# Optimization experiments

Hardware: AMD Instinct MI355X
Metric: run time of the kernel (lower is better)

## Reference

```python
import jax, jax.numpy as jnp
import numpy as np

NUM_HEADS = 16
DIM_HEAD = 64
SCALE = DIM_HEAD ** -0.5
ROPE_BASE = 10000.0


def _rope(t):
    # t: [b, h, n, d] -> rotary embedding with rotate-half convention
    n, d = t.shape[2], t.shape[3]
    inv_freq = 1.0 / (ROPE_BASE ** (jnp.arange(0, d, 2, dtype=jnp.float32) / d))
    freqs = jnp.arange(n, dtype=jnp.float32)[:, None] * inv_freq[None, :]  # [n, d/2]
    cos = jnp.concatenate([jnp.cos(freqs), jnp.cos(freqs)], axis=-1)  # [n, d]
    sin = jnp.concatenate([jnp.sin(freqs), jnp.sin(freqs)], axis=-1)
    t1, t2 = jnp.split(t, 2, axis=-1)
    rot = jnp.concatenate([-t2, t1], axis=-1)
    return t * cos + rot * sin


def setup_inputs() -> dict:
    key = jax.random.key(0)
    k1, k2, k3 = jax.random.split(key, 3)
    B, N, D = 2, 2049, 1024  # 2048 patches + 1 cls token
    x = jax.random.normal(k1, (B, N, D), dtype=jnp.float32)
    ln_gamma = jnp.ones((D,), dtype=jnp.float32)
    ln_beta = jnp.zeros((D,), dtype=jnp.float32)
    w_qkv = jax.random.normal(k2, (D, 3 * NUM_HEADS * DIM_HEAD), dtype=jnp.float32) * 0.02
    w_out = jax.random.normal(k3, (NUM_HEADS * DIM_HEAD, D), dtype=jnp.float32) * 0.02
    return {"x": x, "ln_gamma": ln_gamma, "ln_beta": ln_beta, "w_qkv": w_qkv, "w_out": w_out}


def reference(x, ln_gamma, ln_beta, w_qkv, w_out):
    B, N, D = x.shape
    # LayerNorm (eps=1e-5, torch default)
    mu = jnp.mean(x, axis=-1, keepdims=True)
    var = jnp.mean(jnp.square(x - mu), axis=-1, keepdims=True)
    xn = (x - mu) * jax.lax.rsqrt(var + 1e-5) * ln_gamma + ln_beta
    # QKV projection (no bias)
    qkv = xn @ w_qkv  # [B, N, 3*H*Dh]
    q, k, v = jnp.split(qkv, 3, axis=-1)
    def to_heads(t):
        return t.reshape(B, N, NUM_HEADS, DIM_HEAD).transpose(0, 2, 1, 3)  # [B,H,N,Dh]
    q, k, v = to_heads(q), to_heads(k), to_heads(v)
    # cls token excluded from RoPE
    q = jnp.concatenate([q[:, :, :1, :], _rope(q[:, :, 1:, :])], axis=2)
    k = jnp.concatenate([k[:, :, :1, :], _rope(k[:, :, 1:, :])], axis=2)
    dots = jnp.einsum('bhqd,bhkd->bhqk', q, k) * SCALE
    attn = jax.nn.softmax(dots, axis=-1)
    out = jnp.einsum('bhqk,bhkd->bhqd', attn, v)
    out = out.transpose(0, 2, 1, 3).reshape(B, N, NUM_HEADS * DIM_HEAD)
    return out @ w_out
```

## Files before the change

### kernel.cpp

```cpp
#include <hip/hip_runtime.h>

#define B_    2
#define N_    2049
#define NPAD  2112
#define D_    1024
#define H_    16
#define DH    64
#define MROWS (B_ * N_)
#define MPAD  4224
#define QSCALE 0.18033688011117674f

using bf16x8 = __attribute__((ext_vector_type(8))) short;
using f32x4  = __attribute__((ext_vector_type(4))) float;
using f32x16 = __attribute__((ext_vector_type(16))) float;

#define AS1 __attribute__((address_space(1)))
#define AS3 __attribute__((address_space(3)))

__device__ __forceinline__ float bf2f(short s) {
  union { unsigned u; float f; } a; a.u = ((unsigned)(unsigned short)s) << 16; return a.f;
}
__device__ __forceinline__ short f2bf(float f) {
  union { float f; unsigned u; } a; a.f = f;
  unsigned r = a.u + 0x7fffu + ((a.u >> 16) & 1u);
  return (short)(r >> 16);
}
__device__ __forceinline__ unsigned pack_trunc(float lo, float hi) {
  union { float f; unsigned u; } a, b; a.f = lo; b.f = hi;
  return (b.u & 0xffff0000u) | (a.u >> 16);
}
__device__ __forceinline__ float hexp2(float x) { return __builtin_amdgcn_exp2f(x); }
__device__ __forceinline__ void dma16(const short* g, AS3 short* l) {
  __builtin_amdgcn_global_load_lds((const AS1 unsigned*)g, (AS3 unsigned*)l, 16, 0, 0);
}

__device__ __forceinline__ size_t tiled_off(int m, int k) {
  return ((size_t)(m >> 7) << 17)
       + (size_t)(((k >> 5) << 12)
       + ((((m & 127) >> 4)) << 9)
       + (((((m & 15) << 2) | ((k & 31) >> 3))) << 3)
       + (k & 7));
}

__global__ __launch_bounds__(256) void prep_kernel(const float* __restrict__ x,
                                                   const float* __restrict__ gamma,
                                                   const float* __restrict__ beta,
                                                   short* __restrict__ xn,
                                                   const float* __restrict__ w_qkv,
                                                   short* __restrict__ wqkvT,
                                                   const float* __restrict__ w_out,
                                                   short* __restrict__ woutT) {
  int blk = blockIdx.x;
  int tid = threadIdx.x;
  __shared__ float T[64][65];
  __shared__ float sb[4], s2b[4];

  if (blk < MROWS) {
    int row = blk;
    const float4 v = ((const float4*)(x + (size_t)row * D_))[tid];
    float s  = v.x + v.y + v.z + v.w;
    float ss = v.x * v.x + v.y * v.y + v.z * v.z + v.w * v.w;
    for (int o = 1; o < 64; o <<= 1) { s += __shfl_xor(s, o, 64); ss += __shfl_xor(ss, o, 64); }
    int wid = tid >> 6;
    if ((tid & 63) == 0) { sb[wid] = s; s2b[wid] = ss; }
    __syncthreads();
    float st  = sb[0] + sb[1] + sb[2] + sb[3];
    float sst = s2b[0] + s2b[1] + s2b[2] + s2b[3];
    float mu  = st * (1.0f / D_);
    float var = sst * (1.0f / D_) - mu * mu;
    float rs  = rsqrtf(var + 1e-5f);
    const float4 g  = ((const float4*)gamma)[tid];
    const float4 be = ((const float4*)beta)[tid];
    short4 o4;
    o4.x = f2bf((v.x - mu) * rs * g.x + be.x);
    o4.y = f2bf((v.y - mu) * rs * g.y + be.y);
    o4.z = f2bf((v.z - mu) * rs * g.z + be.z);
    o4.w = f2bf((v.w - mu) * rs * g.w + be.w);
    *(short4*)(xn + tiled_off(row, tid * 4)) = o4;
    return;
  }

  const float* in; short* out; int Nn, t2;
  int b2 = blk - MROWS;
  if (b2 < 768) { in = w_qkv; out = wqkvT; Nn = 3072; t2 = b2; }
  else          { in = w_out; out = woutT; Nn = 1024; t2 = b2 - 768; }
  int k0 = (t2 & 15) * 64;
  int n0 = (t2 >> 4) * 64;
  int r = tid >> 2, c0 = (tid & 3) * 16;
  const float* ip = in + (size_t)(k0 + r) * Nn + n0 + c0;
  #pragma unroll
  for (int j = 0; j < 4; ++j) {
    float4 v = *(const float4*)(ip + j * 4);
    T[r][c0 + j * 4 + 0] = v.x; T[r][c0 + j * 4 + 1] = v.y;
    T[r][c0 + j * 4 + 2] = v.z; T[r][c0 + j * 4 + 3] = v.w;
  }
  __syncthreads();
  bf16x8 w0, w1;
  #pragma unroll
  for (int j = 0; j < 8; ++j) {
    w0[j] = f2bf(T[c0 + j][r]);
    w1[j] = f2bf(T[c0 + 8 + j][r]);
  }
  *(bf16x8*)(out + tiled_off(n0 + r, k0 + c0))     = w0;
  *(bf16x8*)(out + tiled_off(n0 + r, k0 + c0 + 8)) = w1;
}

#define BM 128
#define BK 32
template <typename OutT>
__global__ __launch_bounds__(256) void gemm128(const short* __restrict__ A,
                                               const short* __restrict__ BT,
                                               OutT* __restrict__ C,
                                               int Mstore, int Ncols, int K) {
  int lane = threadIdx.x & 63, wid = threadIdx.x >> 6;
  int quad = lane >> 4, l16 = lane & 15;
  int wr = wid >> 1, wc = wid & 1;
  int m0 = blockIdx.x * BM;
  int n0 = blockIdx.y * BM;

  __shared__ __align__(16) short Abuf[2][BM * BK];
  __shared__ __align__(16) short Bbuf[2][BM * BK];
  AS3 short* AbufL = (AS3 short*)&Abuf[0][0];
  AS3 short* BbufL = (AS3 short*)&Bbuf[0][0];

  f32x4 acc[4][4] = {};

  const short* Ap = A  + ((size_t)(m0 >> 7) << 17);
  const short* Bp = BT + ((size_t)(n0 >> 7) << 17);

  auto stage = [&](int kt, int bb) {
    #pragma unroll
    for (int i = 0; i < 2; ++i) {
      int j = wid * 2 + i;
      dma16(Ap + ((size_t)kt << 12) + j * 512 + lane * 8, AbufL + bb * (BM * BK) + j * 512);
      dma16(Bp + ((size_t)kt << 12) + j * 512 + lane * 8, BbufL + bb * (BM * BK) + j * 512);
    }
  };

  stage(0, 0);
  __syncthreads();

  int KT = K / BK;
  for (int kt = 0; kt < KT; ++kt) {
    int cur = kt & 1;
    if (kt + 1 < KT) stage(kt + 1, cur ^ 1);
    const short* Ab = &Abuf[cur][0];
    const short* Bb = &Bbuf[cur][0];
    bf16x8 af[4], bfr[4];
    #pragma unroll
    for (int s = 0; s < 4; ++s)
      af[s] = *(const bf16x8*)&Ab[(wr * 64 + s * 16 + l16) * BK + quad * 8];
    #pragma unroll
    for (int t = 0; t < 4; ++t)
      bfr[t] = *(const bf16x8*)&Bb[(wc * 64 + t * 16 + l16) * BK + quad * 8];
    #pragma unroll
    for (int s = 0; s < 4; ++s)
      #pragma unroll
      for (int t = 0; t < 4; ++t)
        acc[s][t] = __builtin_amdgcn_mfma_f32_16x16x32_bf16(af[s], bfr[t], acc[s][t], 0, 0, 0);
    __syncthreads();
  }

  #pragma unroll
  for (int s = 0; s < 4; ++s)
    #pragma unroll
    for (int r = 0; r < 4; ++r) {
      int row = m0 + wr * 64 + s * 16 + quad * 4 + r;
      if (row < Mstore) {
        size_t rb = (size_t)row * Ncols + n0 + wc * 64;
        #pragma unroll
        for (int t = 0; t < 4; ++t) {
          float val = acc[s][t][r];
          if constexpr (sizeof(OutT) == 2)
            C[rb + t * 16 + l16] = (OutT)(unsigned short)f2bf(val);
          else
            C[rb + t * 16 + l16] = (OutT)val;
        }
      }
    }
}

__global__ __launch_bounds__(256) void rope_kernel(const short* __restrict__ qkv,
                                                   short* __restrict__ qg,
                                                   short* __restrict__ kfrag,
                                                   short* __restrict__ vfrag) {
  int bh = blockIdx.y;
  int n0 = blockIdx.x * 64;
  int b = bh >> 4, h = bh & 15;
  int t = threadIdx.x;
  int nl = t >> 2;
  int p  = t & 3;
  int n  = n0 + nl;
  size_t hb = (size_t)bh * NPAD * DH;
  size_t ob = hb + (size_t)n * DH;

  __shared__ short Vt[64][66];
  __shared__ short Kt[64][66];

  bf16x8 oq1 = {}, oq2 = {}, ok1 = {}, ok2 = {};
  short v1s[8] = {}, v2s[8] = {};
  if (n < N_) {
    size_t ib = ((size_t)(b * N_ + n)) * 3072 + h * DH;
    bf16x8 q1v = *(const bf16x8*)(qkv + ib + p * 8);
    bf16x8 q2v = *(const bf16x8*)(qkv + ib + 32 + p * 8);
    bf16x8 k1v = *(const bf16x8*)(qkv + ib + 1024 + p * 8);
    bf16x8 k2v = *(const bf16x8*)(qkv + ib + 1024 + 32 + p * 8);
    bf16x8 v1v = *(const bf16x8*)(qkv + ib + 2048 + p * 8);
    bf16x8 v2v = *(const bf16x8*)(qkv + ib + 2048 + 32 + p * 8);
    #pragma unroll
    for (int j = 0; j < 8; ++j) {
      int i = p * 8 + j;
      float q1 = bf2f(q1v[j]), q2 = bf2f(q2v[j]);
      float k1 = bf2f(k1v[j]), k2 = bf2f(k2v[j]);
      if (n > 0) {
        float ang = (float)(n - 1) * hexp2((float)i * -0.4152410118609203f);
        float rev = ang * 0.15915494309189535f;
        rev = rev - floorf(rev);
        float sn = __builtin_amdgcn_sinf(rev);
        float cs = __builtin_amdgcn_cosf(rev);
        float nq1 = q1 * cs - q2 * sn, nq2 = q2 * cs + q1 * sn;
        float nk1 = k1 * cs - k2 * sn, nk2 = k2 * cs + k1 * sn;
        q1 = nq1; q2 = nq2; k1 = nk1; k2 = nk2;
      }
      oq1[j] = f2bf(q1 * QSCALE); oq2[j] = f2bf(q2 * QSCALE);
      ok1[j] = f2bf(k1); ok2[j] = f2bf(k2);
      v1s[j] = v1v[j]; v2s[j] = v2v[j];
    }
  }
  *(bf16x8*)(qg + ob + p * 8)      = oq1;
  *(bf16x8*)(qg + ob + 32 + p * 8) = oq2;
  #pragma unroll
  for (int j = 0; j < 8; ++j) {
    Vt[nl][p * 8 + j]      = v1s[j];
    Vt[nl][32 + p * 8 + j] = v2s[j];
    Kt[nl][p * 8 + j]      = ok1[j];
    Kt[nl][32 + p * 8 + j] = ok2[j];
  }
  __syncthreads();

  int l = t & 63, c = t >> 6;
  int lk = l & 31, hi = l >> 5;
  size_t tb = hb + (size_t)(n0 >> 6) * 4096;
  bf16x8 wv0, wv1, wk0, wk1;
  #pragma unroll
  for (int i = 0; i < 8; ++i) {
    int keyr = c * 16 + hi * 8 + i;
    wv0[i] = Vt[keyr][lk];
    wv1[i] = Vt[keyr][32 + lk];
    wk0[i] = Kt[lk][keyr];
    wk1[i] = Kt[32 + lk][keyr];
  }
  *(bf16x8*)(vfrag + tb + (size_t)(0 * 4 + c) * 512 + l * 8) = wv0;
  *(bf16x8*)(vfrag + tb + (size_t)(4 + c) * 512 + l * 8)     = wv1;
  *(bf16x8*)(kfrag + tb + (size_t)(0 * 4 + c) * 512 + l * 8) = wk0;
  *(bf16x8*)(kfrag + tb + (size_t)(4 + c) * 512 + l * 8)     = wk1;
}

__global__ __launch_bounds__(256, 3) void attn_kernel(const short* __restrict__ qg,
                                                      const short* __restrict__ kfrag,
                                                      const short* __restrict__ vfrag,
                                                      short* __restrict__ Opart,
                                                      float* __restrict__ lpart) {
  int blk = blockIdx.x;
  int xcd = blk & 7;
  int t_  = blk >> 3;
  int bh  = xcd * 4 + (t_ & 3);
  int u   = t_ >> 2;
  int ks  = (u >= 17) ? 1 : 0;
  int qblk = u - ks * 17;
  int kt0 = ks * 17, kt1 = ks ? 32 : 16;

  int lane = threadIdx.x & 63, wid = threadIdx.x >> 6;
  int q    = lane & 31;
  int half = lane >> 5;
  int q0   = qblk * 128 + wid * 32;
  size_t hb = (size_t)bh * NPAD * DH;
  const short* kf_hb = kfrag + hb;
  const short* vf_hb = vfrag + hb;

  __shared__ __align__(16) short Kbuf[3][8 * 512];
  AS3 short* KbufL = (AS3 short*)&Kbuf[0][0];
  const short* KbufR = &Kbuf[0][0];

  int qr = q0 + q; if (qr >= NPAD) qr = 0;
  const short* qp = qg + hb + (size_t)qr * DH + half * 8;
  bf16x8 qf[4];
  #pragma unroll
  for (int s = 0; s < 4; ++s) qf[s] = *(const bf16x8*)(qp + s * 16);

  f32x16 o0 = {}, o1 = {};
  float lrun = 0.0f;

  auto stage = [&](int kt, int bb) {
    const short* src = kf_hb + (size_t)kt * 4096;
    #pragma unroll
    for (int i = 0; i < 2; ++i) {
      int j = wid * 2 + i;
      dma16(src + j * 512 + lane * 8, KbufL + bb * 4096 + j * 512);
    }
  };

  stage(kt0, 0);
  stage(kt0 + 1, 1);

  for (int kt = kt0; kt <= kt1; ++kt) {
    int rb = (kt - kt0) % 3;
    int k0 = kt * 64;

    asm volatile("s_waitcnt vmcnt(2)" ::: "memory");
    __builtin_amdgcn_s_barrier();

    const short* vt = vf_hb + (size_t)kt * 4096;
    bf16x8 vf0[4], vf1[4];
    #pragma unroll
    for (int s = 0; s < 4; ++s) {
      vf0[s] = *(const bf16x8*)(vt + (0 * 4 + s) * 512 + lane * 8);
      vf1[s] = *(const bf16x8*)(vt + (4 + s) * 512 + lane * 8);
    }
    __builtin_amdgcn_sched_barrier(0);
    if (kt + 2 <= kt1) stage(kt + 2, (kt - kt0 + 2) % 3);
    __builtin_amdgcn_sched_barrier(0);

    const short* Kc = KbufR + rb * 4096;
    f32x16 sA = {}, sB = {};
    __builtin_amdgcn_s_setprio(1);
    #pragma unroll
    for (int s = 0; s < 4; ++s) {
      bf16x8 kf0 = *(const bf16x8*)&Kc[(0 * 4 + s) * 512 + lane * 8];
      bf16x8 kf1 = *(const bf16x8*)&Kc[(1 * 4 + s) * 512 + lane * 8];
      sA = __builtin_amdgcn_mfma_f32_32x32x16_bf16(kf0, qf[s], sA, 0, 0, 0);
      sB = __builtin_amdgcn_mfma_f32_32x32x16_bf16(kf1, qf[s], sB, 0, 0, 0);
    }
    __builtin_amdgcn_s_setprio(0);

    if (k0 + 64 > N_) {
      #pragma unroll
      for (int rr = 0; rr < 16; ++rr) {
        int key = (rr & 3) + 8 * (rr >> 2) + 4 * half;
        if (k0 + key >= N_)      sA[rr] = -1e30f;
        if (k0 + 32 + key >= N_) sB[rr] = -1e30f;
      }
    }

    float vsum = 0.0f;
    #pragma unroll
    for (int rr = 0; rr < 16; ++rr) {
      sA[rr] = hexp2(sA[rr]); vsum += sA[rr];
      sB[rr] = hexp2(sB[rr]); vsum += sB[rr];
    }
    lrun += vsum;

    unsigned w[4][4];
    #pragma unroll
    for (int g = 0; g < 2; ++g) {
      #pragma unroll
      for (int fs = 0; fs < 2; ++fs) {
        int b0 = fs * 8;
        float e0, e1, e2, e3, e4, e5, e6, e7;
        if (g == 0) {
          e0 = sA[b0+0]; e1 = sA[b0+1]; e2 = sA[b0+2]; e3 = sA[b0+3];
          e4 = sA[b0+4]; e5 = sA[b0+5]; e6 = sA[b0+6]; e7 = sA[b0+7];
        } else {
          e0 = sB[b0+0]; e1 = sB[b0+1]; e2 = sB[b0+2]; e3 = sB[b0+3];
          e4 = sB[b0+4]; e5 = sB[b0+5]; e6 = sB[b0+6]; e7 = sB[b0+7];
        }
        unsigned X1 = pack_trunc(e0, e1);
        unsigned X2 = pack_trunc(e2, e3);
        unsigned Y1 = pack_trunc(e4, e5);
        unsigned Y2 = pack_trunc(e6, e7);
        asm("v_permlane32_swap_b32 %0, %1" : "+v"(X1), "+v"(Y1));
        asm("v_permlane32_swap_b32 %0, %1" : "+v"(X2), "+v"(Y2));
        int kst = g * 2 + fs;
        w[kst][0] = X1; w[kst][1] = X2; w[kst][2] = Y1; w[kst][3] = Y2;
      }
    }

    __builtin_amdgcn_s_setprio(1);
    #pragma unroll
    for (int kst = 0; kst < 4; ++kst) {
      union { unsigned u[4]; bf16x8 v; } bw;
      bw.u[0] = w[kst][0]; bw.u[1] = w[kst][1]; bw.u[2] = w[kst][2]; bw.u[3] = w[kst][3];
      o0 = __builtin_amdgcn_mfma_f32_32x32x16_bf16(vf0[kst], bw.v, o0, 0, 0, 0);
      o1 = __builtin_amdgcn_mfma_f32_32x32x16_bf16(vf1[kst], bw.v, o1, 0, 0, 0);
    }
    __builtin_amdgcn_s_setprio(0);
  }

  lrun += __shfl_xor(lrun, 32, 64);

  int qrow = q0 + q;
  if (qrow < N_) {
    size_t ob = (((size_t)ks * 32 + bh) * NPAD + qrow) * 64;
    #pragma unroll
    for (int m = 0; m < 2; ++m) {
      #pragma unroll
      for (int gq = 0; gq < 4; ++gq) {
        float a0 = m ? o1[gq*4+0] : o0[gq*4+0];
        float a1 = m ? o1[gq*4+1] : o0[gq*4+1];
        float a2 = m ? o1[gq*4+2] : o0[gq*4+2];
        float a3 = m ? o1[gq*4+3] : o0[gq*4+3];
        short4 st;
        st.x = f2bf(a0); st.y = f2bf(a1); st.z = f2bf(a2); st.w = f2bf(a3);
        int dh = m * 32 + gq * 8 + half * 4;
        *(short4*)(Opart + ob + dh) = st;
      }
    }
    if (half == 0) lpart[((size_t)ks * 32 + bh) * NPAD + qrow] = lrun;
  }
}

__global__ __launch_bounds__(256) void combine_kernel(const short* __restrict__ Opart,
                                                      const float* __restrict__ lpart,
                                                      short* __restrict__ attn_out) {
  int idx = blockIdx.x * 256 + threadIdx.x;
  const int total = 32 * N_ * 16;
  if (idx >= total) return;
  int c4 = idx & 15;
  int t = idx >> 4;
  int n = t % N_;
  int bh = t / N_;
  int b = bh >> 4, h = bh & 15;
  const size_t halfO = (size_t)32 * NPAD * 64;
  size_t off = ((size_t)bh * NPAD + n) * 64 + c4 * 4;
  short4 a  = *(const short4*)(Opart + off);
  short4 bb = *(const short4*)(Opart + halfO + off);
  float la = lpart[(size_t)bh * NPAD + n];
  float lb = lpart[(size_t)32 * NPAD + (size_t)bh * NPAD + n];
  float inv = 1.0f / (la + lb);
  short4 st;
  st.x = f2bf((bf2f(a.x) + bf2f(bb.x)) * inv);
  st.y = f2bf((bf2f(a.y) + bf2f(bb.y)) * inv);
  st.z = f2bf((bf2f(a.z) + bf2f(bb.z)) * inv);
  st.w = f2bf((bf2f(a.w) + bf2f(bb.w)) * inv);
  *(short4*)(attn_out + tiled_off(b * N_ + n, h * DH + c4 * 4)) = st;
}

extern "C" void kernel_launch(void* const* d_in, const int* in_sizes, int n_in,
                              void* d_out, int out_size, void* d_ws, size_t ws_size,
                              hipStream_t stream) {
  const float* x     = (const float*)d_in[0];
  const float* gamma = (const float*)d_in[1];
  const float* beta  = (const float*)d_in[2];
  const float* w_qkv = (const float*)d_in[3];
  const float* w_out = (const float*)d_in[4];

  short* wqkvT = (short*)d_ws;
  short* woutT = wqkvT + (size_t)3072 * 1024;
  short* xn    = woutT + (size_t)1024 * 1024;
  short* qkv   = xn    + (size_t)MPAD * 1024;
  short* qg    = qkv   + (size_t)MPAD * 3072;
  short* kfragG = qg    + (size_t)B_ * H_ * NPAD * DH;
  short* vfragG = kfragG + (size_t)B_ * H_ * NPAD * DH;
  short* attn_out = xn;
  short* Opart = qkv;
  float* lpart = (float*)(qkv + (size_t)2 * 32 * NPAD * 64);

  prep_kernel<<<MROWS + 768 + 256, 256, 0, stream>>>(x, gamma, beta, xn,
                                                     w_qkv, wqkvT, w_out, woutT);
  {
    dim3 g(MPAD / 128, 3072 / 128);
    gemm128<unsigned short><<<g, 256, 0, stream>>>(xn, wqkvT, (unsigned short*)qkv, MROWS, 3072, 1024);
  }
  {
    dim3 g(33, 32);
    rope_kernel<<<g, 256, 0, stream>>>(qkv, qg, kfragG, vfragG);
  }
  attn_kernel<<<8 * 4 * 17 * 2, 256, 0, stream>>>(qg, kfragG, vfragG, Opart, lpart);
  combine_kernel<<<(32 * N_ * 16 + 255) / 256, 256, 0, stream>>>(Opart, lpart, attn_out);
  {
    dim3 g(MPAD / 128, 1024 / 128);
    gemm128<float><<<g, 256, 0, stream>>>(attn_out, woutT, (float*)d_out, MROWS, 1024, 1024);
  }
}
```

Before: 231.9 us.

## Stage V tiles through LDS via async DMA and swizzle GEMM blocks across XCDs

Measured after the change: 225.6 us. 2.7% less time.

```diff
diff --git a/kernel.cpp b/kernel.cpp
--- a/kernel.cpp
+++ b/kernel.cpp
@@ -115,8 +115,11 @@
   int lane = threadIdx.x & 63, wid = threadIdx.x >> 6;
   int quad = lane >> 4, l16 = lane & 15;
   int wr = wid >> 1, wc = wid & 1;
-  int m0 = blockIdx.x * BM;
-  int n0 = blockIdx.y * BM;
+  int chunk = gridDim.x >> 3;
+  int swz = (blockIdx.x & 7) * chunk + (blockIdx.x >> 3);
+  int mb = swz % 33, nb = swz / 33;
+  int m0 = mb * BM;
+  int n0 = nb * BM;
 
   __shared__ __align__(16) short Abuf[2][BM * BK];
   __shared__ __align__(16) short Bbuf[2][BM * BK];
@@ -278,9 +281,12 @@
   const short* kf_hb = kfrag + hb;
   const short* vf_hb = vfrag + hb;
 
-  __shared__ __align__(16) short Kbuf[3][8 * 512];
+  __shared__ __align__(16) short Kbuf[3][4096];
+  __shared__ __align__(16) short Vbuf[3][4096];
   AS3 short* KbufL = (AS3 short*)&Kbuf[0][0];
+  AS3 short* VbufL = (AS3 short*)&Vbuf[0][0];
   const short* KbufR = &Kbuf[0][0];
+  const short* VbufR = &Vbuf[0][0];
 
   int qr = q0 + q; if (qr >= NPAD) qr = 0;
   const short* qp = qg + hb + (size_t)qr * DH + half * 8;
@@ -292,11 +298,13 @@
   float lrun = 0.0f;
 
   auto stage = [&](int kt, int bb) {
-    const short* src = kf_hb + (size_t)kt * 4096;
+    const short* ksrc = kf_hb + (size_t)kt * 4096;
+    const short* vsrc = vf_hb + (size_t)kt * 4096;
     #pragma unroll
     for (int i = 0; i < 2; ++i) {
       int j = wid * 2 + i;
-      dma16(src + j * 512 + lane * 8, KbufL + bb * 4096 + j * 512);
+      dma16(ksrc + j * 512 + lane * 8, KbufL + bb * 4096 + j * 512);
+      dma16(vsrc + j * 512 + lane * 8, VbufL + bb * 4096 + j * 512);
     }
   };
 
@@ -307,19 +315,19 @@
     int rb = (kt - kt0) % 3;
     int k0 = kt * 64;
 
-    asm volatile("s_waitcnt vmcnt(2)" ::: "memory");
+    asm volatile("s_waitcnt vmcnt(4)" ::: "memory");
     __builtin_amdgcn_s_barrier();
 
-    const short* vt = vf_hb + (size_t)kt * 4096;
-    bf16x8 vf0[4], vf1[4];
-    #pragma unroll
-    for (int s = 0; s < 4; ++s) {
-      vf0[s] = *(const bf16x8*)(vt + (0 * 4 + s) * 512 + lane * 8);
-      vf1[s] = *(const bf16x8*)(vt + (4 + s) * 512 + lane * 8);
-    }
-    __builtin_amdgcn_sched_barrier(0);
     if (kt + 2 <= kt1) stage(kt + 2, (kt - kt0 + 2) % 3);
     __builtin_amdgcn_sched_barrier(0);
+
+    const short* Vc = VbufR + rb * 4096;
+    bf16x8 vf0[4], vf1[4];
+    #pragma unroll
+    for (int s = 0; s < 4; ++s) {
+      vf0[s] = *(const bf16x8*)&Vc[(0 * 4 + s) * 512 + lane * 8];
+      vf1[s] = *(const bf16x8*)&Vc[(4 + s) * 512 + lane * 8];
+    }
 
     const short* Kc = KbufR + rb * 4096;
     f32x16 sA = {}, sB = {};
@@ -457,18 +465,12 @@
 
   prep_kernel<<<MROWS + 768 + 256, 256, 0, stream>>>(x, gamma, beta, xn,
                                                      w_qkv, wqkvT, w_out, woutT);
-  {
-    dim3 g(MPAD / 128, 3072 / 128);
-    gemm128<unsigned short><<<g, 256, 0, stream>>>(xn, wqkvT, (unsigned short*)qkv, MROWS, 3072, 1024);
-  }
+  gemm128<unsigned short><<<792, 256, 0, stream>>>(xn, wqkvT, (unsigned short*)qkv, MROWS, 3072, 1024);
   {
     dim3 g(33, 32);
     rope_kernel<<<g, 256, 0, stream>>>(qkv, qg, kfragG, vfragG);
   }
   attn_kernel<<<8 * 4 * 17 * 2, 256, 0, stream>>>(qg, kfragG, vfragG, Opart, lpart);
   combine_kernel<<<(32 * N_ * 16 + 255) / 256, 256, 0, stream>>>(Opart, lpart, attn_out);
-  {
-    dim3 g(MPAD / 128, 1024 / 128);
-    gemm128<float><<<g, 256, 0, stream>>>(attn_out, woutT, (float*)d_out, MROWS, 1024, 1024);
-  }
-}
+  gemm128<float><<<264, 256, 0, stream>>>(attn_out, woutT, (float*)d_out, MROWS, 1024, 1024);
+}
```
